# Kernel optimization log

Measured on AMD Instinct MI355X. Metric: run time of the kernel, lower is better.

Reference implementation:

```python
import jax, jax.numpy as jnp
import numpy as np

B, S, K, M, U, C = 4096, 512, 10, 20, 256, 128
BIAS = 0.0  # args.b
OSC_TIME = 5


def _ff(xin, h, jxW, jxb, jhW, jhb, kxW, kxb, khW, khb):
    # FF gated cell: out = j*(1-h) + (1-k)*h
    j = jax.nn.sigmoid(xin @ jxW + jxb + h @ jhW + jhb)
    k = jax.nn.sigmoid(xin @ kxW + kxb + h @ khW + khb)
    return j * (1.0 - h) + (1.0 - k) * h


def setup_inputs() -> dict:
    key = jax.random.key(0)
    ks = iter(jax.random.split(key, 48))
    def rn(shape, scale=0.05):
        return jax.random.normal(next(ks), shape, dtype=jnp.float32) * scale
    inp = {}
    inp["x"] = rn((B, 1, 3), 1.0)
    inp["c_vec"] = rn((B, U, C), 1.0)
    inp["rnn_1_h"] = jnp.zeros((B, S), jnp.float32)
    inp["rnn_2_h"] = jnp.zeros((B, S), jnp.float32)
    inp["osc_h"] = jnp.zeros((4, B, S), jnp.float32)  # [phi, omega, r, mu] states
    inp["init_w"] = jnp.zeros((B, 1, C), jnp.float32)
    inp["init_kappa"] = jnp.zeros((B, K, 1), jnp.float32)
    for nm, din in (("r1", 3 + C), ("r2", 3 + S + C)):
        for g in ("j", "k"):
            inp[nm + "_" + g + "x_W"] = rn((din, S))
            inp[nm + "_" + g + "x_b"] = jnp.zeros((S,), jnp.float32)
            inp[nm + "_" + g + "h_W"] = rn((S, S))
            inp[nm + "_" + g + "h_b"] = jnp.zeros((S,), jnp.float32)
    for g in ("j", "k"):
        inp["osc_" + g + "x_W"] = rn((4, S, S))
        inp["osc_" + g + "x_b"] = jnp.zeros((4, S), jnp.float32)
        inp["osc_" + g + "h_W"] = rn((4, S, S))
        inp["osc_" + g + "h_b"] = jnp.zeros((4, S), jnp.float32)
    inp["win_W"] = rn((S, 3 * K))
    inp["win_b"] = jnp.zeros((3 * K,), jnp.float32)
    inp["lin_W"] = rn((S, 1 + 6 * M))
    inp["lin_b"] = jnp.zeros((1 + 6 * M,), jnp.float32)
    return inp


def reference(x, c_vec, rnn_1_h, rnn_2_h, osc_h, init_w, init_kappa,
              r1_jx_W, r1_jx_b, r1_jh_W, r1_jh_b, r1_kx_W, r1_kx_b, r1_kh_W, r1_kh_b,
              r2_jx_W, r2_jx_b, r2_jh_W, r2_jh_b, r2_kx_W, r2_kx_b, r2_kh_W, r2_kh_b,
              osc_jx_W, osc_jx_b, osc_jh_W, osc_jh_b, osc_kx_W, osc_kx_b, osc_kh_W, osc_kh_b,
              win_W, win_b, lin_W, lin_b):
    # ---- rnn1 over a single timestep ----
    in1 = jnp.concatenate([x, init_w], axis=2)[:, 0]  # [B, 3+C]
    h1 = _ff(in1, rnn_1_h, r1_jx_W, r1_jx_b, r1_jh_W, r1_jh_b,
             r1_kx_W, r1_kx_b, r1_kh_W, r1_kh_b)  # [B,S]
    # ---- Gaussian window attention over character sequence ----
    kg = h1 @ win_W + win_b  # [B,3K]
    alpha_hat, beta_hat, kappa_hat = jnp.split(kg, 3, axis=1)
    alpha = jnp.exp(alpha_hat)[:, :, None]  # [B,K,1]
    beta = jnp.exp(beta_hat)[:, :, None]
    kappa = init_kappa + jnp.exp(kappa_hat)[:, :, None]  # [B,K,1]
    u = jnp.arange(U, dtype=jnp.float32)  # [U]
    phi = jnp.sum(jnp.exp(jnp.square(kappa - u) * -beta) * alpha, axis=1, keepdims=True)  # [B,1,U]
    w = jnp.squeeze(phi @ c_vec, 1)  # [B,C]
    # ---- rnn2 ----
    in2 = jnp.concatenate([x[:, 0], h1, w], axis=1)  # [B, 3+S+C]
    h2 = _ff(in2, rnn_2_h, r2_jx_W, r2_jx_b, r2_jh_W, r2_jh_b,
             r2_kx_W, r2_kx_b, r2_kh_W, r2_kh_b)  # [B,S]
    # ---- FFOsc: 4 gated cells (phi, omega, r, mu) computed batched over n=4 ----
    j = jax.nn.sigmoid(jnp.einsum('bs,nst->nbt', h2, osc_jx_W) + osc_jx_b[:, None, :]
                       + jnp.einsum('nbs,nst->nbt', osc_h, osc_jh_W) + osc_jh_b[:, None, :])
    k = jax.nn.sigmoid(jnp.einsum('bs,nst->nbt', h2, osc_kx_W) + osc_kx_b[:, None, :]
                       + jnp.einsum('nbs,nst->nbt', osc_h, osc_kh_W) + osc_kh_b[:, None, :])
    osc_new = j * (1.0 - osc_h) + (1.0 - k) * osc_h  # [4,B,S]
    phi_o, omega_o, r_o, mu_o = osc_new[0], osc_new[1], osc_new[2], osc_new[3]
    # explicit oscillator recurrence, OSC_TIME=5 steps
    zs = [r_o * jnp.cos(phi_o)]
    for _ in range(OSC_TIME - 1):
        r_o = r_o + (mu_o - jnp.square(r_o)) * r_o
        phi_o = phi_o + omega_o
        zs.append(r_o * jnp.cos(phi_o))
    osc_out = jnp.stack(zs, axis=1)  # [B,5,S]
    # ---- MDN head ----
    out = osc_out.reshape(-1, S) @ lin_W + lin_b  # [B*5, 1+6M]
    eos = 1.0 / (1.0 + jnp.exp(out[:, 0]))
    pi_hat, mu1, mu2, s1_hat, s2_hat, rho_hat = jnp.split(out[:, 1:], 6, axis=1)
    pi = jax.nn.softmax(pi_hat * (1.0 + BIAS), axis=1)
    sigma1 = jnp.exp(s1_hat - BIAS)
    sigma2 = jnp.exp(s2_hat - BIAS)
    rho = jnp.tanh(rho_hat)
    return (eos, pi, mu1, mu2, sigma1, sigma2, rho, h1, h2, osc_new, w, phi, kappa)
```

## Files before the change

### kernel.cpp

```cpp
#include <hip/hip_runtime.h>
#include <math.h>

#define BB_ 4096
#define SS_ 512
#define KK_ 10
#define MM_ 20
#define UU_ 256
#define CC_ 128

#define EOS_OFF   0
#define PI_OFF    20480
#define MU1_OFF   430080
#define MU2_OFF   839680
#define S1_OFF    1249280
#define S2_OFF    1658880
#define RHO_OFF   2068480
#define H1_OFF    2478080
#define H2_OFF    4575232
#define OSC_OFF   6672384
#define W_OFF     15060992
#define PHI_OFF   15585280
#define KAPPA_OFF 16633856

#define KP1 672
#define KP2 1184
#define KPO 1024

typedef __attribute__((ext_vector_type(8))) short s8b;
typedef __attribute__((ext_vector_type(4))) float f4;

__device__ __forceinline__ float sigmoidf_(float x) {
    return 1.0f / (1.0f + __expf(-x));
}

__device__ __forceinline__ unsigned short f2b(float v) {
    union { float f; unsigned int u; } c; c.f = v;
    unsigned int r = (c.u + 0x7FFFu + ((c.u >> 16) & 1u)) >> 16;
    return (unsigned short)r;
}

__global__ __launch_bounds__(256) void pack_x1(
    const float* __restrict__ x, const float* __restrict__ init_w,
    const float* __restrict__ h, unsigned short* __restrict__ X)
{
    int idx = blockIdx.x * 256 + threadIdx.x;
    if (idx >= BB_ * KP1) return;
    int b = idx / KP1, c = idx - b * KP1;
    float v = 0.0f;
    if (c < 3)        v = x[b * 3 + c];
    else if (c < 131) v = init_w[b * 128 + (c - 3)];
    else if (c < 643) v = h[b * 512 + (c - 131)];
    X[idx] = f2b(v);
}

__global__ __launch_bounds__(256) void pack_x2(
    const float* __restrict__ x, const float* __restrict__ h1,
    const float* __restrict__ w, const float* __restrict__ h2p,
    unsigned short* __restrict__ X)
{
    int idx = blockIdx.x * 256 + threadIdx.x;
    if (idx >= BB_ * KP2) return;
    int b = idx / KP2, c = idx - b * KP2;
    float v = 0.0f;
    if (c < 3)         v = x[b * 3 + c];
    else if (c < 515)  v = h1[b * 512 + (c - 3)];
    else if (c < 643)  v = w[b * 128 + (c - 515)];
    else if (c < 1155) v = h2p[b * 512 + (c - 643)];
    X[idx] = f2b(v);
}

__global__ __launch_bounds__(256) void pack_xosc(
    const float* __restrict__ h2, const float* __restrict__ osc_h,
    unsigned short* __restrict__ X)
{
    int idx = blockIdx.x * 256 + threadIdx.x;
    int c = idx & 1023;
    int b = (idx >> 10) & 4095;
    int z = idx >> 22;
    float v = (c < 512) ? h2[b * 512 + c]
                        : osc_h[((size_t)z * BB_ + b) * 512 + (c - 512)];
    X[idx] = f2b(v);
}

__global__ __launch_bounds__(256) void pack_w(
    const float* __restrict__ src_x, int d1, size_t sxz,
    const float* __restrict__ src_h, size_t shz,
    unsigned short* __restrict__ dst, int Kp, size_t dz)
{
    __shared__ float t[32][65];
    const int tid = threadIdx.x;
    const int nc0 = blockIdx.x * 64;
    const int k0 = blockIdx.y * 32;
    const int z = blockIdx.z;
    const float* sx = src_x + (size_t)z * sxz;
    const float* sh = src_h + (size_t)z * shz;
    unsigned short* dd = dst + (size_t)z * dz;

    for (int i = tid; i < 64 * 32; i += 256) {
        int ncl = i & 63, kl = i >> 6;
        int k = k0 + kl;
        float v = 0.0f;
        if (k < d1)            v = sx[(size_t)k * 512 + nc0 + ncl];
        else if (k < d1 + 512) v = sh[(size_t)(k - d1) * 512 + nc0 + ncl];
        t[kl][ncl] = v;
    }
    __syncthreads();
    for (int i = tid; i < 64 * 32; i += 256) {
        int kl = i & 31, ncl = i >> 5;
        dd[(size_t)(nc0 + ncl) * Kp + k0 + kl] = f2b(t[kl][ncl]);
    }
}

__global__ __launch_bounds__(256) void gemm_gate(
    const unsigned short* __restrict__ A, size_t az, int Kp,
    const unsigned short* __restrict__ Wj, const unsigned short* __restrict__ Wk, size_t wz,
    const float* __restrict__ jxb, const float* __restrict__ jhb,
    const float* __restrict__ kxb, const float* __restrict__ khb,
    const float* __restrict__ h_prev, size_t hz,
    float* __restrict__ out, size_t oz)
{
    __shared__ unsigned short As[128 * 40];
    __shared__ unsigned short Bjs[128 * 40];
    __shared__ unsigned short Bks[128 * 40];

    const int tid = threadIdx.x;
    const int lane = tid & 63;
    const int w = tid >> 6;
    const int wr = w >> 1, wc = w & 1;
    const int b0 = blockIdx.x * 128;
    const int s0 = blockIdx.y * 128;
    const int z = blockIdx.z;

    const unsigned short* Az = A + (size_t)z * az;
    const unsigned short* Wjz = Wj + (size_t)z * wz;
    const unsigned short* Wkz = Wk + (size_t)z * wz;

    f4 accj[4][4], acck[4][4];
#pragma unroll
    for (int m = 0; m < 4; m++)
#pragma unroll
        for (int c = 0; c < 4; c++) {
            accj[m][c] = (f4)0.0f;
            acck[m][c] = (f4)0.0f;
        }

    const int lr = lane & 15;
    const int ks = (lane >> 4) * 8;
    const int nK = Kp >> 5;

    for (int kt = 0; kt < nK; kt++) {
        const int k0 = kt * 32;
#pragma unroll
        for (int i = tid; i < 512; i += 256) {
            int row = i >> 2, seg = i & 3;
            *(uint4*)&As[row * 40 + seg * 8] =
                *(const uint4*)(Az + (size_t)(b0 + row) * Kp + k0 + seg * 8);
            *(uint4*)&Bjs[row * 40 + seg * 8] =
                *(const uint4*)(Wjz + (size_t)(s0 + row) * Kp + k0 + seg * 8);
            *(uint4*)&Bks[row * 40 + seg * 8] =
                *(const uint4*)(Wkz + (size_t)(s0 + row) * Kp + k0 + seg * 8);
        }
        __syncthreads();

        s8b af[4], bjf[4], bkf[4];
#pragma unroll
        for (int m = 0; m < 4; m++)
            af[m] = *(const s8b*)&As[(wr * 64 + m * 16 + lr) * 40 + ks];
#pragma unroll
        for (int c = 0; c < 4; c++) {
            bjf[c] = *(const s8b*)&Bjs[(wc * 64 + c * 16 + lr) * 40 + ks];
            bkf[c] = *(const s8b*)&Bks[(wc * 64 + c * 16 + lr) * 40 + ks];
        }
#pragma unroll
        for (int m = 0; m < 4; m++)
#pragma unroll
            for (int c = 0; c < 4; c++) {
                accj[m][c] = __builtin_amdgcn_mfma_f32_16x16x32_bf16(af[m], bjf[c], accj[m][c], 0, 0, 0);
                acck[m][c] = __builtin_amdgcn_mfma_f32_16x16x32_bf16(af[m], bkf[c], acck[m][c], 0, 0, 0);
            }
        __syncthreads();
    }

    const float* hp = h_prev + (size_t)z * hz;
    float* op = out + (size_t)z * oz;
    const int zb = z * 512;
#pragma unroll
    for (int c = 0; c < 4; c++) {
        const int scol = s0 + wc * 64 + c * 16 + lr;
        const float bj = jxb[zb + scol] + jhb[zb + scol];
        const float bk = kxb[zb + scol] + khb[zb + scol];
#pragma unroll
        for (int m = 0; m < 4; m++) {
            const int r0 = b0 + wr * 64 + m * 16 + (lane >> 4) * 4;
#pragma unroll
            for (int reg = 0; reg < 4; reg++) {
                const int r = r0 + reg;
                const float h = hp[(size_t)r * 512 + scol];
                const float jv = sigmoidf_(accj[m][c][reg] + bj);
                const float kv = sigmoidf_(acck[m][c][reg] + bk);
                op[(size_t)r * 512 + scol] = jv * (1.0f - h) + (1.0f - kv) * h;
            }
        }
    }
}

__global__ __launch_bounds__(256) void win_kernel(
    const float* __restrict__ h1,
    const float* __restrict__ winW, const float* __restrict__ winb,
    const float* __restrict__ init_kappa,
    const float* __restrict__ c_vec,
    float* __restrict__ out)
{
    __shared__ float hl[512];
    __shared__ float part[8][30];
    __shared__ float kg[30];
    __shared__ float alpha_s[10], beta_s[10], kap_s[10];
    __shared__ float phil[256];
    __shared__ float wpart[256];

    const int tid = threadIdx.x;
    const int b = blockIdx.x;

    hl[tid] = h1[b * 512 + tid];
    hl[256 + tid] = h1[b * 512 + 256 + tid];
    __syncthreads();

    if (tid < 240) {
        int c = tid % 30, p = tid / 30;
        float a = 0.0f;
        int s0 = p * 64;
#pragma unroll 4
        for (int i = 0; i < 64; i++) a = fmaf(hl[s0 + i], winW[(s0 + i) * 30 + c], a);
        part[p][c] = a;
    }
    __syncthreads();
    if (tid < 30) {
        float a = winb[tid];
#pragma unroll
        for (int p = 0; p < 8; p++) a += part[p][tid];
        kg[tid] = a;
    }
    __syncthreads();
    if (tid < 10) {
        alpha_s[tid] = __expf(kg[tid]);
        beta_s[tid] = __expf(kg[10 + tid]);
        float kp = init_kappa[b * 10 + tid] + __expf(kg[20 + tid]);
        kap_s[tid] = kp;
        out[KAPPA_OFF + b * 10 + tid] = kp;
    }
    __syncthreads();
    {
        float u = (float)tid;
        float p = 0.0f;
#pragma unroll
        for (int k = 0; k < 10; k++) {
            float d = kap_s[k] - u;
            p += alpha_s[k] * __expf(-beta_s[k] * d * d);
        }
        phil[tid] = p;
        out[PHI_OFF + b * 256 + tid] = p;
    }
    __syncthreads();
    {
        int c = tid & 127, half = tid >> 7;
        const float* cv = c_vec + (size_t)b * UU_ * CC_ + (size_t)half * 128 * CC_ + c;
        float a = 0.0f;
#pragma unroll 4
        for (int uu = 0; uu < 128; uu++) a = fmaf(phil[half * 128 + uu], cv[uu * CC_], a);
        wpart[tid] = a;
    }
    __syncthreads();
    if (tid < 128) out[W_OFF + b * CC_ + tid] = wpart[tid] + wpart[128 + tid];
}

__global__ __launch_bounds__(256) void mdn_kernel(
    const float* __restrict__ osc_new,
    const float* __restrict__ linW, const float* __restrict__ linb,
    float* __restrict__ out)
{
    __shared__ float zl[20][512];
    __shared__ float ol[20][121];
    const int tid = threadIdx.x;
    const int b0 = blockIdx.x * 4;

    for (int idx = tid; idx < 4 * 512; idx += 256) {
        int bb = idx >> 9, sI = idx & 511;
        int b = b0 + bb;
        float ph = osc_new[((size_t)0 * BB_ + b) * SS_ + sI];
        float om = osc_new[((size_t)1 * BB_ + b) * SS_ + sI];
        float r  = osc_new[((size_t)2 * BB_ + b) * SS_ + sI];
        float mu = osc_new[((size_t)3 * BB_ + b) * SS_ + sI];
        zl[bb * 5 + 0][sI] = r * __cosf(ph);
#pragma unroll
        for (int tt = 1; tt < 5; tt++) {
            r = fmaf(mu - r * r, r, r);
            ph += om;
            zl[bb * 5 + tt][sI] = r * __cosf(ph);
        }
    }
    __syncthreads();

    if (tid < 242) {
        int c = tid % 121, rh = tid / 121;
        float acc[10];
        const float lb = linb[c];
#pragma unroll
        for (int rr = 0; rr < 10; rr++) acc[rr] = lb;
#pragma unroll 4
        for (int s = 0; s < 512; s++) {
            float wv = linW[s * 121 + c];
#pragma unroll
            for (int rr = 0; rr < 10; rr++)
                acc[rr] = fmaf(zl[rh * 10 + rr][s], wv, acc[rr]);
        }
#pragma unroll
        for (int rr = 0; rr < 10; rr++) ol[rh * 10 + rr][c] = acc[rr];
    }
    __syncthreads();

    if (tid < 20) {
        const int row = tid;
        const int rg = b0 * 5 + row;
        const float* o = ol[row];
        out[EOS_OFF + rg] = 1.0f / (1.0f + __expf(o[0]));
        float mx = -1e30f;
#pragma unroll
        for (int m = 0; m < 20; m++) mx = fmaxf(mx, o[1 + m]);
        float ex[20];
        float sum = 0.0f;
#pragma unroll
        for (int m = 0; m < 20; m++) { ex[m] = __expf(o[1 + m] - mx); sum += ex[m]; }
        float inv = 1.0f / sum;
#pragma unroll
        for (int m = 0; m < 20; m++) {
            out[PI_OFF  + rg * 20 + m] = ex[m] * inv;
            out[MU1_OFF + rg * 20 + m] = o[21 + m];
            out[MU2_OFF + rg * 20 + m] = o[41 + m];
            out[S1_OFF  + rg * 20 + m] = __expf(o[61 + m]);
            out[S2_OFF  + rg * 20 + m] = __expf(o[81 + m]);
            out[RHO_OFF + rg * 20 + m] = tanhf(o[101 + m]);
        }
    }
}

extern "C" void kernel_launch(void* const* d_in, const int* in_sizes, int n_in,
                              void* d_out, int out_size, void* d_ws, size_t ws_size,
                              hipStream_t stream)
{
    const float* x          = (const float*)d_in[0];
    const float* c_vec      = (const float*)d_in[1];
    const float* rnn_1_h    = (const float*)d_in[2];
    const float* rnn_2_h    = (const float*)d_in[3];
    const float* osc_h      = (const float*)d_in[4];
    const float* init_w     = (const float*)d_in[5];
    const float* init_kappa = (const float*)d_in[6];
    const float* r1_jx_W = (const float*)d_in[7];
    const float* r1_jx_b = (const float*)d_in[8];
    const float* r1_jh_W = (const float*)d_in[9];
    const float* r1_jh_b = (const float*)d_in[10];
    const float* r1_kx_W = (const float*)d_in[11];
    const float* r1_kx_b = (const float*)d_in[12];
    const float* r1_kh_W = (const float*)d_in[13];
    const float* r1_kh_b = (const float*)d_in[14];
    const float* r2_jx_W = (const float*)d_in[15];
    const float* r2_jx_b = (const float*)d_in[16];
    const float* r2_jh_W = (const float*)d_in[17];
    const float* r2_jh_b = (const float*)d_in[18];
    const float* r2_kx_W = (const float*)d_in[19];
    const float* r2_kx_b = (const float*)d_in[20];
    const float* r2_kh_W = (const float*)d_in[21];
    const float* r2_kh_b = (const float*)d_in[22];
    const float* osc_jx_W = (const float*)d_in[23];
    const float* osc_jx_b = (const float*)d_in[24];
    const float* osc_jh_W = (const float*)d_in[25];
    const float* osc_jh_b = (const float*)d_in[26];
    const float* osc_kx_W = (const float*)d_in[27];
    const float* osc_kx_b = (const float*)d_in[28];
    const float* osc_kh_W = (const float*)d_in[29];
    const float* osc_kh_b = (const float*)d_in[30];
    const float* win_W = (const float*)d_in[31];
    const float* win_b = (const float*)d_in[32];
    const float* lin_W = (const float*)d_in[33];
    const float* lin_b = (const float*)d_in[34];

    float* out = (float*)d_out;
    unsigned short* ws = (unsigned short*)d_ws;

    unsigned short* X1   = ws;
    unsigned short* X2   = X1 + (size_t)BB_ * KP1;
    unsigned short* Xo   = X2 + (size_t)BB_ * KP2;
    unsigned short* Wj1  = Xo + (size_t)4 * BB_ * KPO;
    unsigned short* Wk1  = Wj1 + (size_t)512 * KP1;
    unsigned short* Wj2  = Wk1 + (size_t)512 * KP1;
    unsigned short* Wk2  = Wj2 + (size_t)512 * KP2;
    unsigned short* WjO  = Wk2 + (size_t)512 * KP2;
    unsigned short* WkO  = WjO + (size_t)4 * 512 * KPO;

    pack_w<<<dim3(8, KP1 / 32, 1), 256, 0, stream>>>(r1_jx_W, 131, 0, r1_jh_W, 0, Wj1, KP1, 0);
    pack_w<<<dim3(8, KP1 / 32, 1), 256, 0, stream>>>(r1_kx_W, 131, 0, r1_kh_W, 0, Wk1, KP1, 0);
    pack_w<<<dim3(8, KP2 / 32, 1), 256, 0, stream>>>(r2_jx_W, 643, 0, r2_jh_W, 0, Wj2, KP2, 0);
    pack_w<<<dim3(8, KP2 / 32, 1), 256, 0, stream>>>(r2_kx_W, 643, 0, r2_kh_W, 0, Wk2, KP2, 0);
    pack_w<<<dim3(8, KPO / 32, 4), 256, 0, stream>>>(osc_jx_W, 512, (size_t)512 * 512, osc_jh_W, (size_t)512 * 512, WjO, KPO, (size_t)512 * KPO);
    pack_w<<<dim3(8, KPO / 32, 4), 256, 0, stream>>>(osc_kx_W, 512, (size_t)512 * 512, osc_kh_W, (size_t)512 * 512, WkO, KPO, (size_t)512 * KPO);

    pack_x1<<<(BB_ * KP1 + 255) / 256, 256, 0, stream>>>(x, init_w, rnn_1_h, X1);
    gemm_gate<<<dim3(32, 4, 1), 256, 0, stream>>>(
        X1, 0, KP1, Wj1, Wk1, 0,
        r1_jx_b, r1_jh_b, r1_kx_b, r1_kh_b,
        rnn_1_h, 0, out + H1_OFF, 0);

    win_kernel<<<BB_, 256, 0, stream>>>(out + H1_OFF, win_W, win_b,
                                        init_kappa, c_vec, out);

    pack_x2<<<(BB_ * KP2 + 255) / 256, 256, 0, stream>>>(x, out + H1_OFF, out + W_OFF, rnn_2_h, X2);
    gemm_gate<<<dim3(32, 4, 1), 256, 0, stream>>>(
        X2, 0, KP2, Wj2, Wk2, 0,
        r2_jx_b, r2_jh_b, r2_kx_b, r2_kh_b,
        rnn_2_h, 0, out + H2_OFF, 0);

    pack_xosc<<<(4 * BB_ * KPO) / 256, 256, 0, stream>>>(out + H2_OFF, osc_h, Xo);
    gemm_gate<<<dim3(32, 4, 4), 256, 0, stream>>>(
        Xo, (size_t)BB_ * KPO, KPO, WjO, WkO, (size_t)512 * KPO,
        osc_jx_b, osc_jh_b, osc_kx_b, osc_kh_b,
        osc_h, (size_t)BB_ * SS_, out + OSC_OFF, (size_t)BB_ * SS_);

    mdn_kernel<<<BB_ / 4, 256, 0, stream>>>(out + OSC_OFF, lin_W, lin_b, out);
}
```

Baseline: 1.204 ms.

## Move MDN head matmul to bf16 MFMA and vectorize pack_xosc and win reduction

Rewrites the MDN head so the oscillator-unrolled activations and a transposed, zero-padded bf16 copy of lin_W are staged in shared memory and multiplied with 16x16x32 bf16 MFMA instructions. Each block now handles 16 batch rows instead of 4, and the bias is added in the epilogue. This replaces the scalar fp32 FMA loop that recomputed per block. It also widens pack_xosc to 8 elements per thread with 128-bit stores, and vectorizes the c_vec weighted sum in win_kernel with float4 loads over 8 u-groups. The trade-off is bf16 rounding of the MDN inputs and weights, plus an extra weight-packing launch.

Result: faster. 1.095 ms (-9.0%).

```diff
diff --git a/kernel.cpp b/kernel.cpp
--- a/kernel.cpp
+++ b/kernel.cpp
@@ -73,13 +73,18 @@
     const float* __restrict__ h2, const float* __restrict__ osc_h,
     unsigned short* __restrict__ X)
 {
-    int idx = blockIdx.x * 256 + threadIdx.x;
-    int c = idx & 1023;
-    int b = (idx >> 10) & 4095;
-    int z = idx >> 22;
-    float v = (c < 512) ? h2[b * 512 + c]
-                        : osc_h[((size_t)z * BB_ + b) * 512 + (c - 512)];
-    X[idx] = f2b(v);
+    int t = blockIdx.x * 256 + threadIdx.x;
+    int c0 = (t << 3) & 1023;
+    int b = (t >> 7) & 4095;
+    int z = t >> 19;
+    const float* src = (c0 < 512) ? h2 + (size_t)b * 512 + c0
+                                  : osc_h + ((size_t)z * BB_ + b) * 512 + (c0 - 512);
+    f4 v0 = *(const f4*)src;
+    f4 v1 = *(const f4*)(src + 4);
+    union { unsigned short u[8]; uint4 q; } o;
+    o.u[0] = f2b(v0.x); o.u[1] = f2b(v0.y); o.u[2] = f2b(v0.z); o.u[3] = f2b(v0.w);
+    o.u[4] = f2b(v1.x); o.u[5] = f2b(v1.y); o.u[6] = f2b(v1.z); o.u[7] = f2b(v1.w);
+    *(uint4*)&X[(size_t)t * 8] = o.q;
 }
 
 __global__ __launch_bounds__(256) void pack_w(
@@ -111,6 +116,25 @@
     }
 }
 
+__global__ __launch_bounds__(256) void pack_lin(
+    const float* __restrict__ linW, unsigned short* __restrict__ Wl)
+{
+    __shared__ float t[32][65];
+    const int tid = threadIdx.x;
+    const int n0 = blockIdx.x * 64;
+    const int k0 = blockIdx.y * 32;
+    for (int i = tid; i < 64 * 32; i += 256) {
+        int ncl = i & 63, kl = i >> 6;
+        int n = n0 + ncl;
+        t[kl][ncl] = (n < 121) ? linW[(size_t)(k0 + kl) * 121 + n] : 0.0f;
+    }
+    __syncthreads();
+    for (int i = tid; i < 64 * 32; i += 256) {
+        int kl = i & 31, ncl = i >> 5;
+        Wl[(size_t)(n0 + ncl) * 512 + k0 + kl] = f2b(t[kl][ncl]);
+    }
+}
+
 __global__ __launch_bounds__(256) void gemm_gate(
     const unsigned short* __restrict__ A, size_t az, int Kp,
     const unsigned short* __restrict__ Wj, const unsigned short* __restrict__ Wk, size_t wz,
@@ -216,7 +240,7 @@
     __shared__ float kg[30];
     __shared__ float alpha_s[10], beta_s[10], kap_s[10];
     __shared__ float phil[256];
-    __shared__ float wpart[256];
+    __shared__ f4 wacc[8][32];
 
     const int tid = threadIdx.x;
     const int b = blockIdx.x;
@@ -262,83 +286,130 @@
     }
     __syncthreads();
     {
-        int c = tid & 127, half = tid >> 7;
-        const float* cv = c_vec + (size_t)b * UU_ * CC_ + (size_t)half * 128 * CC_ + c;
-        float a = 0.0f;
+        const int c4 = tid & 31, ug = tid >> 5;
+        const f4* cv4 = (const f4*)(c_vec + (size_t)b * UU_ * CC_);
+        f4 a4 = (f4)0.0f;
 #pragma unroll 4
-        for (int uu = 0; uu < 128; uu++) a = fmaf(phil[half * 128 + uu], cv[uu * CC_], a);
-        wpart[tid] = a;
-    }
-    __syncthreads();
-    if (tid < 128) out[W_OFF + b * CC_ + tid] = wpart[tid] + wpart[128 + tid];
+        for (int i = 0; i < 32; i++) {
+            int u = ug * 32 + i;
+            f4 v = cv4[(size_t)u * 32 + c4];
+            float p = phil[u];
+            a4 += v * p;
+        }
+        wacc[ug][c4] = a4;
+    }
+    __syncthreads();
+    if (tid < 32) {
+        f4 s = wacc[0][tid];
+#pragma unroll
+        for (int g = 1; g < 8; g++) s += wacc[g][tid];
+        *(f4*)(out + W_OFF + (size_t)b * CC_ + tid * 4) = s;
+    }
 }
 
 __global__ __launch_bounds__(256) void mdn_kernel(
     const float* __restrict__ osc_new,
-    const float* __restrict__ linW, const float* __restrict__ linb,
+    const unsigned short* __restrict__ Wl, const float* __restrict__ linb,
     float* __restrict__ out)
 {
-    __shared__ float zl[20][512];
-    __shared__ float ol[20][121];
+    __shared__ float epi[80][133];
+    __shared__ float lbs[121];
+    unsigned short* As = (unsigned short*)&epi[0][0];
+    unsigned short* Bs = As + 80 * 40;
+
     const int tid = threadIdx.x;
-    const int b0 = blockIdx.x * 4;
-
-    for (int idx = tid; idx < 4 * 512; idx += 256) {
-        int bb = idx >> 9, sI = idx & 511;
-        int b = b0 + bb;
-        float ph = osc_new[((size_t)0 * BB_ + b) * SS_ + sI];
-        float om = osc_new[((size_t)1 * BB_ + b) * SS_ + sI];
-        float r  = osc_new[((size_t)2 * BB_ + b) * SS_ + sI];
-        float mu = osc_new[((size_t)3 * BB_ + b) * SS_ + sI];
-        zl[bb * 5 + 0][sI] = r * __cosf(ph);
-#pragma unroll
-        for (int tt = 1; tt < 5; tt++) {
-            r = fmaf(mu - r * r, r, r);
-            ph += om;
-            zl[bb * 5 + tt][sI] = r * __cosf(ph);
-        }
-    }
-    __syncthreads();
-
-    if (tid < 242) {
-        int c = tid % 121, rh = tid / 121;
-        float acc[10];
-        const float lb = linb[c];
-#pragma unroll
-        for (int rr = 0; rr < 10; rr++) acc[rr] = lb;
-#pragma unroll 4
-        for (int s = 0; s < 512; s++) {
-            float wv = linW[s * 121 + c];
-#pragma unroll
-            for (int rr = 0; rr < 10; rr++)
-                acc[rr] = fmaf(zl[rh * 10 + rr][s], wv, acc[rr]);
-        }
-#pragma unroll
-        for (int rr = 0; rr < 10; rr++) ol[rh * 10 + rr][c] = acc[rr];
-    }
-    __syncthreads();
-
-    if (tid < 20) {
-        const int row = tid;
-        const int rg = b0 * 5 + row;
-        const float* o = ol[row];
-        out[EOS_OFF + rg] = 1.0f / (1.0f + __expf(o[0]));
+    const int lane = tid & 63;
+    const int w = tid >> 6;
+    const int lr = lane & 15;
+    const int ks = (lane >> 4) * 8;
+    const int b0 = blockIdx.x * 16;
+
+    if (tid < 121) lbs[tid] = linb[tid];
+
+    f4 acc[5][2];
+#pragma unroll
+    for (int m = 0; m < 5; m++)
+#pragma unroll
+        for (int n = 0; n < 2; n++) acc[m][n] = (f4)0.0f;
+
+    for (int kt = 0; kt < 16; kt++) {
+        const int k0 = kt * 32;
+#pragma unroll
+        for (int t = 0; t < 2; t++) {
+            int task = tid + t * 256;
+            int bl = task >> 5, sl = task & 31;
+            int b = b0 + bl, s = k0 + sl;
+            float ph = osc_new[(size_t)0 * BB_ * SS_ + (size_t)b * SS_ + s];
+            float om = osc_new[(size_t)1 * BB_ * SS_ + (size_t)b * SS_ + s];
+            float r  = osc_new[(size_t)2 * BB_ * SS_ + (size_t)b * SS_ + s];
+            float mu = osc_new[(size_t)3 * BB_ * SS_ + (size_t)b * SS_ + s];
+            As[(bl * 5 + 0) * 40 + sl] = f2b(r * __cosf(ph));
+#pragma unroll
+            for (int tt = 1; tt < 5; tt++) {
+                r = fmaf(mu - r * r, r, r);
+                ph += om;
+                As[(bl * 5 + tt) * 40 + sl] = f2b(r * __cosf(ph));
+            }
+        }
+#pragma unroll
+        for (int i = tid; i < 512; i += 256) {
+            int row = i >> 2, seg = i & 3;
+            *(uint4*)&Bs[row * 40 + seg * 8] =
+                *(const uint4*)(Wl + (size_t)row * 512 + k0 + seg * 8);
+        }
+        __syncthreads();
+
+        s8b a[5], bf[2];
+#pragma unroll
+        for (int m = 0; m < 5; m++)
+            a[m] = *(const s8b*)&As[(m * 16 + lr) * 40 + ks];
+#pragma unroll
+        for (int n = 0; n < 2; n++)
+            bf[n] = *(const s8b*)&Bs[(w * 32 + n * 16 + lr) * 40 + ks];
+#pragma unroll
+        for (int m = 0; m < 5; m++)
+#pragma unroll
+            for (int n = 0; n < 2; n++)
+                acc[m][n] = __builtin_amdgcn_mfma_f32_16x16x32_bf16(a[m], bf[n], acc[m][n], 0, 0, 0);
+        __syncthreads();
+    }
+
+#pragma unroll
+    for (int m = 0; m < 5; m++)
+#pragma unroll
+        for (int n = 0; n < 2; n++) {
+            const int col = w * 32 + n * 16 + lr;
+#pragma unroll
+            for (int reg = 0; reg < 4; reg++) {
+                const int row = m * 16 + (lane >> 4) * 4 + reg;
+                epi[row][col] = acc[m][n][reg];
+            }
+        }
+    __syncthreads();
+
+    if (tid < 80) {
+        const int rg = b0 * 5 + tid;
+        const float* o = epi[tid];
+        out[EOS_OFF + rg] = 1.0f / (1.0f + __expf(o[0] + lbs[0]));
         float mx = -1e30f;
-#pragma unroll
-        for (int m = 0; m < 20; m++) mx = fmaxf(mx, o[1 + m]);
-        float ex[20];
+        float pv[20];
+#pragma unroll
+        for (int m = 0; m < 20; m++) {
+            pv[m] = o[1 + m] + lbs[1 + m];
+            mx = fmaxf(mx, pv[m]);
+        }
         float sum = 0.0f;
 #pragma unroll
-        for (int m = 0; m < 20; m++) { ex[m] = __expf(o[1 + m] - mx); sum += ex[m]; }
+        for (int m = 0; m < 20; m++) { pv[m] = __expf(pv[m] - mx); sum += pv[m]; }
         float inv = 1.0f / sum;
 #pragma unroll
         for (int m = 0; m < 20; m++) {
-            out[PI_OFF  + rg * 20 + m] = ex[m] * inv;
-            out[MU1_OFF + rg * 20 + m] = o[21 + m];
-            out[MU2_OFF + rg * 20 + m] = o[41 + m];
-            out[S1_OFF  + rg * 20 + m] = __expf(o[61 + m]);
-            out[S2_OFF  + rg * 20 + m] = __expf(o[81 + m]);
-            out[RHO_OFF + rg * 20 + m] = tanhf(o[101 + m]);
+            out[PI_OFF  + rg * 20 + m] = pv[m] * inv;
+            out[MU1_OFF + rg * 20 + m] = o[21 + m] + lbs[21 + m];
+            out[MU2_OFF + rg * 20 + m] = o[41 + m] + lbs[41 + m];
+            out[S1_OFF  + rg * 20 + m] = __expf(o[61 + m] + lbs[61 + m]);
+            out[S2_OFF  + rg * 20 + m] = __expf(o[81 + m] + lbs[81 + m]);
+            out[RHO_OFF + rg * 20 + m] = tanhf(o[101 + m] + lbs[101 + m]);
         }
     }
 }
@@ -395,6 +466,7 @@
     unsigned short* Wk2  = Wj2 + (size_t)512 * KP2;
     unsigned short* WjO  = Wk2 + (size_t)512 * KP2;
     unsigned short* WkO  = WjO + (size_t)4 * 512 * KPO;
+    unsigned short* Wl   = WkO + (size_t)4 * 512 * KPO;
 
     pack_w<<<dim3(8, KP1 / 32, 1), 256, 0, stream>>>(r1_jx_W, 131, 0, r1_jh_W, 0, Wj1, KP1, 0);
     pack_w<<<dim3(8, KP1 / 32, 1), 256, 0, stream>>>(r1_kx_W, 131, 0, r1_kh_W, 0, Wk1, KP1, 0);
@@ -402,6 +474,7 @@
     pack_w<<<dim3(8, KP2 / 32, 1), 256, 0, stream>>>(r2_kx_W, 643, 0, r2_kh_W, 0, Wk2, KP2, 0);
     pack_w<<<dim3(8, KPO / 32, 4), 256, 0, stream>>>(osc_jx_W, 512, (size_t)512 * 512, osc_jh_W, (size_t)512 * 512, WjO, KPO, (size_t)512 * KPO);
     pack_w<<<dim3(8, KPO / 32, 4), 256, 0, stream>>>(osc_kx_W, 512, (size_t)512 * 512, osc_kh_W, (size_t)512 * 512, WkO, KPO, (size_t)512 * KPO);
+    pack_lin<<<dim3(2, 16), 256, 0, stream>>>(lin_W, Wl);
 
     pack_x1<<<(BB_ * KP1 + 255) / 256, 256, 0, stream>>>(x, init_w, rnn_1_h, X1);
     gemm_gate<<<dim3(32, 4, 1), 256, 0, stream>>>(
@@ -418,11 +491,11 @@
         r2_jx_b, r2_jh_b, r2_kx_b, r2_kh_b,
         rnn_2_h, 0, out + H2_OFF, 0);
 
-    pack_xosc<<<(4 * BB_ * KPO) / 256, 256, 0, stream>>>(out + H2_OFF, osc_h, Xo);
+    pack_xosc<<<(4 * BB_ * KPO) / (8 * 256), 256, 0, stream>>>(out + H2_OFF, osc_h, Xo);
     gemm_gate<<<dim3(32, 4, 4), 256, 0, stream>>>(
         Xo, (size_t)BB_ * KPO, KPO, WjO, WkO, (size_t)512 * KPO,
         osc_jx_b, osc_jh_b, osc_kx_b, osc_kh_b,
         osc_h, (size_t)BB_ * SS_, out + OSC_OFF, (size_t)BB_ * SS_);
 
-    mdn_kernel<<<BB_ / 4, 256, 0, stream>>>(out + OSC_OFF, lin_W, lin_b, out);
-}
+    mdn_kernel<<<BB_ / 16, 256, 0, stream>>>(out + OSC_OFF, Wl, lin_b, out);
+}
```
